# Optimization experiments

Hardware: AMD Instinct MI355X
Metric: run time of the kernel (lower is better)

The kernel has to match this reference:

```python
import jax, jax.numpy as jnp
import numpy as np

H = 128   # hidden_size
DYN = 2   # dynamic_features


def setup_inputs() -> dict:
    B, S, STAT = 256, 64, 2
    key = jax.random.key(0)
    ks = jax.random.split(key, 9)
    sc = 0.05
    return {
        "static": jax.random.normal(ks[0], (B, STAT, S), jnp.float32),
        "static_embeddings": jax.random.normal(ks[1], (B, H, S), jnp.float32),
        "dynamic": jax.random.uniform(ks[2], (B, DYN, S), jnp.float32),
        # dynamic_embedding: Conv1d(2 -> 128, k=1)
        "dyn_w": jax.random.normal(ks[3], (H, DYN), jnp.float32) * sc,
        "dyn_b": jnp.zeros((H,), jnp.float32),
        # decoder_input_dynamic_embedding: Conv1d(128 -> 128, k=1)
        "in_w": jax.random.normal(ks[4], (H, H), jnp.float32) * sc,
        "in_b": jnp.zeros((H,), jnp.float32),
        # GRU (single layer, batch_first), torch gate order r,z,n
        "w_ih": jax.random.normal(ks[5], (3 * H, H), jnp.float32) * sc,
        "w_hh": jax.random.normal(ks[6], (3 * H, H), jnp.float32) * sc,
        "b_ih": jnp.zeros((3 * H,), jnp.float32),
        "b_hh": jnp.zeros((3 * H,), jnp.float32),
        # DoubleAttention: scores = v . tanh(W [static; dynamic; hidden])
        "W_att": jax.random.normal(ks[7], (H, 3 * H), jnp.float32) * sc,
        "v_att": jax.random.normal(ks[8], (H,), jnp.float32) * sc,
    }


def _pointer_forward(static_embeddings, dynamic, dyn_w, dyn_b, in_w, in_b,
                     w_ih, w_hh, b_ih, b_hh, W_att, v_att):
    B, Hd, S = static_embeddings.shape
    NEG = jnp.asarray(-1e9, static_embeddings.dtype)
    base = jax.random.key(42)

    def gru_cell(x, h):  # torch nn.GRU single step
        gi = x @ w_ih.T + b_ih
        gh = h @ w_hh.T + b_hh
        ir, iz, i_n = jnp.split(gi, 3, axis=-1)
        hr, hz, h_n = jnp.split(gh, 3, axis=-1)
        r = jax.nn.sigmoid(ir + hr)
        z = jax.nn.sigmoid(iz + hz)
        n = jnp.tanh(i_n + r * h_n)
        return (1.0 - z) * n + z * h

    first_mask = jnp.zeros((B, S), static_embeddings.dtype).at[:, 0].set(1.0)

    def step(carry, i):
        dec_in, h, visited, dyn = carry
        # decoder_input_dynamic_embedding: 1x1 conv == per-token linear
        x = dec_in @ in_w.T + in_b                      # [B,H]
        h = gru_cell(x, h)                              # decoder_output == new hidden
        # i==0: only depot (index 0) is selectable; afterwards: unvisited nodes
        mask = jnp.where(i == 0, first_mask, 1.0 - visited)
        dyn_emb = jnp.einsum('bds,hd->bhs', dyn, dyn_w) + dyn_b[None, :, None]
        ctx = jnp.concatenate(
            [static_embeddings, dyn_emb,
             jnp.broadcast_to(h[:, :, None], (B, Hd, S))], axis=1)  # [B,3H,S]
        scores = jnp.einsum('h,bhs->bs', v_att,
                            jnp.tanh(jnp.einsum('hk,bks->bhs', W_att, ctx)))
        logits = jnp.where(mask > 0, scores, NEG)       # -inf on masked positions
        ptr = jax.random.categorical(jax.random.fold_in(base, i), logits)  # sample
        logp = jnp.take_along_axis(jax.nn.log_softmax(logits, -1),
                                   ptr[:, None], axis=1)[:, 0]
        sel = (jnp.arange(S)[None, :] == ptr[:, None]).astype(dyn.dtype)  # [B,S]
        visited = jnp.maximum(visited, sel)
        dyn = dyn * (1.0 - sel)[:, None, :]             # update_dynamic_state
        # original feeds the (conv-transformed) decoder input back to itself
        return (x, h, visited, dyn), (ptr, logp)

    init = (static_embeddings[:, :, 0],                  # decoder_input = emb of node 0
            jnp.zeros((B, Hd), static_embeddings.dtype),  # GRU hidden
            jnp.zeros((B, S), static_embeddings.dtype),   # visited
            dynamic)
    _, (tours, logps) = jax.lax.scan(step, init, jnp.arange(S))
    return tours.T, logps.T  # [B,S], [B,S]


def reference(static, static_embeddings, dynamic, dyn_w, dyn_b, in_w, in_b,
              w_ih, w_hh, b_ih, b_hh, W_att, v_att):
    # dropout layers are identity in eval mode; `static` is only used for logging
    return _pointer_forward(static_embeddings, dynamic, dyn_w, dyn_b, in_w, in_b,
                            w_ih, w_hh, b_ih, b_hh, W_att, v_att)
```

## Files before the change

### kernel.cpp

```cpp
#include <hip/hip_runtime.h>
#include <stdint.h>


#define BN 256
#define SN 64
#define HN 128
#define NEGV (-1.0e9f)
#define TINYF 1.17549435e-38f

#define OFF_A   0
#define OFF_GI  8192
#define OFF_WHC 8192
#define OFF_SET 16384
#define OFF_UT  24832
#define OFF_HC  33280
#define OFF_KK  33536
#define OFF_SV  33664
#define OFF_DY  33792
#define OFF_WD  33920
#define OFF_CV  34176
#define OFF_VS  34304
#define SMEM_FLOATS 34308

#define KA_A   0
#define KA_GI  8192
#define KA_HC  32768
#define KA_FLOATS 33024

#define WS_HG   384
#define WS_NEED ((size_t)(384 + 256 * 64 * 128) * 4)

typedef float v4f __attribute__((ext_vector_type(4)));

struct W8 { v4f a, b, c, d, e, f, g, h; };

__device__ __forceinline__ W8 ldg8_s64(const float* p) {
  W8 r;
  asm volatile(
      "global_load_dwordx4 %0, %8, off\n\t"
      "global_load_dwordx4 %1, %8, off offset:64\n\t"
      "global_load_dwordx4 %2, %8, off offset:128\n\t"
      "global_load_dwordx4 %3, %8, off offset:192\n\t"
      "global_load_dwordx4 %4, %8, off offset:256\n\t"
      "global_load_dwordx4 %5, %8, off offset:320\n\t"
      "global_load_dwordx4 %6, %8, off offset:384\n\t"
      "global_load_dwordx4 %7, %8, off offset:448\n\t"
      "s_waitcnt vmcnt(0)"
      : "=&v"(r.a), "=&v"(r.b), "=&v"(r.c), "=&v"(r.d),
        "=&v"(r.e), "=&v"(r.f), "=&v"(r.g), "=&v"(r.h)
      : "v"(p));
  return r;
}

__device__ __forceinline__ float dot8(const W8& w, const float4* x4) {
  float a0 = 0.f, a1 = 0.f, a2 = 0.f, a3 = 0.f;
  a0 = fmaf(w.a.x, x4[0].x, a0); a1 = fmaf(w.a.y, x4[0].y, a1);
  a2 = fmaf(w.a.z, x4[0].z, a2); a3 = fmaf(w.a.w, x4[0].w, a3);
  a0 = fmaf(w.b.x, x4[1].x, a0); a1 = fmaf(w.b.y, x4[1].y, a1);
  a2 = fmaf(w.b.z, x4[1].z, a2); a3 = fmaf(w.b.w, x4[1].w, a3);
  a0 = fmaf(w.c.x, x4[2].x, a0); a1 = fmaf(w.c.y, x4[2].y, a1);
  a2 = fmaf(w.c.z, x4[2].z, a2); a3 = fmaf(w.c.w, x4[2].w, a3);
  a0 = fmaf(w.d.x, x4[3].x, a0); a1 = fmaf(w.d.y, x4[3].y, a1);
  a2 = fmaf(w.d.z, x4[3].z, a2); a3 = fmaf(w.d.w, x4[3].w, a3);
  a0 = fmaf(w.e.x, x4[4].x, a0); a1 = fmaf(w.e.y, x4[4].y, a1);
  a2 = fmaf(w.e.z, x4[4].z, a2); a3 = fmaf(w.e.w, x4[4].w, a3);
  a0 = fmaf(w.f.x, x4[5].x, a0); a1 = fmaf(w.f.y, x4[5].y, a1);
  a2 = fmaf(w.f.z, x4[5].z, a2); a3 = fmaf(w.f.w, x4[5].w, a3);
  a0 = fmaf(w.g.x, x4[6].x, a0); a1 = fmaf(w.g.y, x4[6].y, a1);
  a2 = fmaf(w.g.z, x4[6].z, a2); a3 = fmaf(w.g.w, x4[6].w, a3);
  a0 = fmaf(w.h.x, x4[7].x, a0); a1 = fmaf(w.h.y, x4[7].y, a1);
  a2 = fmaf(w.h.z, x4[7].z, a2); a3 = fmaf(w.h.w, x4[7].w, a3);
  return (a0 + a1) + (a2 + a3);
}

__device__ __forceinline__ uint32_t rotl32(uint32_t v, int d) {
  return (v << d) | (v >> (32 - d));
}

__device__ __forceinline__ void threefry2x32(uint32_t k0, uint32_t k1,
                                             uint32_t x0, uint32_t x1,
                                             uint32_t& o0, uint32_t& o1) {
  uint32_t ks2 = k0 ^ k1 ^ 0x1BD11BDAu;
  x0 += k0; x1 += k1;
  x0 += x1; x1 = rotl32(x1, 13); x1 ^= x0;
  x0 += x1; x1 = rotl32(x1, 15); x1 ^= x0;
  x0 += x1; x1 = rotl32(x1, 26); x1 ^= x0;
  x0 += x1; x1 = rotl32(x1, 6);  x1 ^= x0;
  x0 += k1; x1 += ks2 + 1u;
  x0 += x1; x1 = rotl32(x1, 17); x1 ^= x0;
  x0 += x1; x1 = rotl32(x1, 29); x1 ^= x0;
  x0 += x1; x1 = rotl32(x1, 16); x1 ^= x0;
  x0 += x1; x1 = rotl32(x1, 24); x1 ^= x0;
  x0 += ks2; x1 += k0 + 2u;
  x0 += x1; x1 = rotl32(x1, 13); x1 ^= x0;
  x0 += x1; x1 = rotl32(x1, 15); x1 ^= x0;
  x0 += x1; x1 = rotl32(x1, 26); x1 ^= x0;
  x0 += x1; x1 = rotl32(x1, 6);  x1 ^= x0;
  x0 += k0; x1 += k1 + 3u;
  x0 += x1; x1 = rotl32(x1, 17); x1 ^= x0;
  x0 += x1; x1 = rotl32(x1, 29); x1 ^= x0;
  x0 += x1; x1 = rotl32(x1, 16); x1 ^= x0;
  x0 += x1; x1 = rotl32(x1, 24); x1 ^= x0;
  x0 += k1; x1 += ks2 + 4u;
  x0 += x1; x1 = rotl32(x1, 13); x1 ^= x0;
  x0 += x1; x1 = rotl32(x1, 15); x1 ^= x0;
  x0 += x1; x1 = rotl32(x1, 26); x1 ^= x0;
  x0 += x1; x1 = rotl32(x1, 6);  x1 ^= x0;
  x0 += ks2; x1 += k0 + 5u;
  o0 = x0; o1 = x1;
}

__device__ __forceinline__ float jax_gumbel(uint32_t k0, uint32_t k1, int j) {
  uint32_t o0, o1;
  threefry2x32(k0, k1, 0u, (uint32_t)j, o0, o1);
  uint32_t bits = o0 ^ o1;
  uint32_t ub = (bits >> 9) | 0x3F800000u;
  float u = __uint_as_float(ub) - 1.0f;
  u = fmaxf(u + TINYF, TINYF);
  return -logf(-logf(u));
}

__device__ __forceinline__ float ftanh(float x) {
  float e = __expf(2.0f * x);
  return (e - 1.0f) * __builtin_amdgcn_rcpf(e + 1.0f);
}

__device__ __forceinline__ float fsig(float x) {
  return __builtin_amdgcn_rcpf(1.0f + __expf(-x));
}

__global__ void k0_dyn(const float* __restrict__ W_att, const float* __restrict__ dyn_w,
                       const float* __restrict__ dyn_b, float* __restrict__ Wd,
                       float* __restrict__ cv) {
  int h = threadIdx.x;
  float w0 = 0.f, w1 = 0.f, cc = 0.f;
  for (int k = 0; k < HN; ++k) {
    float w = W_att[h * 384 + 128 + k];
    w0 = fmaf(w, dyn_w[2 * k + 0], w0);
    w1 = fmaf(w, dyn_w[2 * k + 1], w1);
    cc = fmaf(w, dyn_b[k], cc);
  }
  Wd[2 * h] = w0; Wd[2 * h + 1] = w1; cv[h] = cc;
}

__global__ __launch_bounds__(512)
__attribute__((amdgpu_waves_per_eu(2, 2)))
void kA_front(const float* __restrict__ SE, const float* __restrict__ in_w,
              const float* __restrict__ in_b, const float* __restrict__ w_ih,
              const float* __restrict__ b_ih, const float* __restrict__ w_hh,
              const float* __restrict__ b_hh, float* __restrict__ Hg) {
  extern __shared__ float sm[];
  float* A   = sm + KA_A;
  float* GIl = sm + KA_GI;
  float* HC  = sm + KA_HC;
  int b = blockIdx.x, t = threadIdx.x;

  if (t < 128) HC[t] = SE[b * 8192 + t * 64];
  __syncthreads();

  {
    int ml = t >> 2, ks = t & 3;
    W8 wv = ldg8_s64(in_w + ml * HN + ks * 4);
    float bib = in_b[ml];
    for (int ii = 0; ii < SN; ++ii) {
      const float* xc = HC + (ii & 1) * 128;
      float* xn = HC + ((ii + 1) & 1) * 128;
      float4 x4[8];
#pragma unroll
      for (int q = 0; q < 8; ++q)
        x4[q] = *(const float4*)(xc + q * 16 + ks * 4);
      float s = dot8(wv, x4);
      s += __shfl_xor(s, 1); s += __shfl_xor(s, 2);
      if (ks == 0) {
        float xv = s + bib;
        A[ii * 128 + ml] = xv;
        xn[ml] = xv;
      }
      __syncthreads();
    }
  }

  {
    int r = t & 127, cg = t >> 7;
    const float* xb = A + cg * 16 * 128;
    const float* w0p = w_ih + (r)       * HN;
    const float* w1p = w_ih + (r + 128) * HN;
    const float* w2p = w_ih + (r + 256) * HN;
    float acc[3][16];
#pragma unroll
    for (int g = 0; g < 3; ++g)
#pragma unroll
      for (int i = 0; i < 16; ++i) acc[g][i] = 0.f;
#pragma unroll 1
    for (int k = 0; k < HN; k += 4) {
      float4 w0 = *(const float4*)(w0p + k);
      float4 w1 = *(const float4*)(w1p + k);
      float4 w2 = *(const float4*)(w2p + k);
#pragma unroll
      for (int i = 0; i < 16; ++i) {
        float4 xv = *(const float4*)(xb + i * 128 + k);
        acc[0][i] = fmaf(w0.x, xv.x, acc[0][i]);
        acc[0][i] = fmaf(w0.y, xv.y, acc[0][i]);
        acc[0][i] = fmaf(w0.z, xv.z, acc[0][i]);
        acc[0][i] = fmaf(w0.w, xv.w, acc[0][i]);
        acc[1][i] = fmaf(w1.x, xv.x, acc[1][i]);
        acc[1][i] = fmaf(w1.y, xv.y, acc[1][i]);
        acc[1][i] = fmaf(w1.z, xv.z, acc[1][i]);
        acc[1][i] = fmaf(w1.w, xv.w, acc[1][i]);
        acc[2][i] = fmaf(w2.x, xv.x, acc[2][i]);
        acc[2][i] = fmaf(w2.y, xv.y, acc[2][i]);
        acc[2][i] = fmaf(w2.z, xv.z, acc[2][i]);
        acc[2][i] = fmaf(w2.w, xv.w, acc[2][i]);
      }
    }
    float b0 = b_ih[r], b1 = b_ih[r + 128], b2 = b_ih[r + 256];
#pragma unroll
    for (int i = 0; i < 16; ++i) {
      int n = cg * 16 + i;
      GIl[n * 384 + r]       = acc[0][i] + b0;
      GIl[n * 384 + 128 + r] = acc[1][i] + b1;
      GIl[n * 384 + 256 + r] = acc[2][i] + b2;
    }
    __syncthreads();
  }

  if (t < 256) HC[t] = 0.f;
  __syncthreads();
  {
    int ml = t >> 2, ks = t & 3;
    W8 wv0 = ldg8_s64(w_hh + (ml)       * HN + ks * 4);
    W8 wv1 = ldg8_s64(w_hh + (ml + 128) * HN + ks * 4);
    W8 wv2 = ldg8_s64(w_hh + (ml + 256) * HN + ks * 4);
    float bh0 = b_hh[ml], bh1 = b_hh[ml + 128], bh2 = b_hh[ml + 256];
    float hp = 0.f;
    for (int ii = 0; ii < SN; ++ii) {
      const float* hcr = HC + (ii & 1) * 128;
      float* hcw = HC + ((ii + 1) & 1) * 128;
      float gi0 = 0.f, gi1 = 0.f, gi2 = 0.f;
      if (ks == 0) {
        const float* gr = GIl + ii * 384;
        gi0 = gr[ml]; gi1 = gr[128 + ml]; gi2 = gr[256 + ml];
      }
      float4 x4[8];
#pragma unroll
      for (int q = 0; q < 8; ++q)
        x4[q] = *(const float4*)(hcr + q * 16 + ks * 4);
      float s0 = dot8(wv0, x4);
      float s1 = dot8(wv1, x4);
      float s2 = dot8(wv2, x4);
      s0 += __shfl_xor(s0, 1); s0 += __shfl_xor(s0, 2);
      s1 += __shfl_xor(s1, 1); s1 += __shfl_xor(s1, 2);
      s2 += __shfl_xor(s2, 1); s2 += __shfl_xor(s2, 2);
      if (ks == 0) {
        float r = fsig(gi0 + s0 + bh0);
        float z = fsig(gi1 + s1 + bh1);
        float nn = ftanh(gi2 + r * (s2 + bh2));
        float hn = (1.0f - z) * nn + z * hp;
        hcw[ml] = hn;
        Hg[b * 8192 + ii * 128 + ml] = hn;
        hp = hn;
      }
      __syncthreads();
    }
  }
}

__global__ __launch_bounds__(1024)
void k3_att(const float* __restrict__ SE, const float* __restrict__ dynamic,
            const float* __restrict__ dyn_w, const float* __restrict__ dyn_b,
            const float* __restrict__ W_att, const float* __restrict__ v_att,
            const float* __restrict__ Hg, float* __restrict__ out) {
  extern __shared__ float sm[];
  int b = blockIdx.x, t = threadIdx.x;
  float* A   = sm + OFF_A;
  float* WHC = sm + OFF_WHC;
  float* SET = sm + OFF_SET;
  float* UT  = sm + OFF_UT;
  uint32_t* KK = (uint32_t*)(sm + OFF_KK);
  float* SV  = sm + OFF_SV;
  float* DY  = sm + OFF_DY;
  float* WDs = sm + OFF_WD;
  float* CVs = sm + OFF_CV;

  if (t < 512) {
    int h = t >> 2, ks2 = t & 3;
    const float* wp = W_att + h * 384 + 128 + ks2 * 32;
    float w0 = 0.f, w1 = 0.f, cc = 0.f;
    for (int k = 0; k < 32; ++k) {
      float w = wp[k];
      int kk = ks2 * 32 + k;
      w0 = fmaf(w, dyn_w[2 * kk + 0], w0);
      w1 = fmaf(w, dyn_w[2 * kk + 1], w1);
      cc = fmaf(w, dyn_b[kk], cc);
    }
    w0 += __shfl_xor(w0, 1); w0 += __shfl_xor(w0, 2);
    w1 += __shfl_xor(w1, 1); w1 += __shfl_xor(w1, 2);
    cc += __shfl_xor(cc, 1); cc += __shfl_xor(cc, 2);
    if (ks2 == 0) { WDs[2 * h] = w0; WDs[2 * h + 1] = w1; CVs[h] = cc; }
  } else if (t < 640) {
    int tt = t - 512;
    SV[tt] = 2.0f * v_att[tt];
    DY[tt] = dynamic[b * 128 + tt];
  } else if (t < 704) {
    int tt = t - 640;
    uint32_t o0, o1;
    threefry2x32(0u, 42u, 0u, (uint32_t)tt, o0, o1);
    KK[2 * tt] = o0; KK[2 * tt + 1] = o1;
  } else if (t < 768) {
    int tt = t - 704;
    float v = v_att[tt] + v_att[tt + 64];
#pragma unroll
    for (int off = 32; off > 0; off >>= 1) v += __shfl_xor(v, off);
    if (tt == 0) sm[OFF_VS] = v;
  }
  for (int p = 0; p < 8; ++p)
    A[p * 1024 + t] = Hg[b * 8192 + p * 1024 + t];
  __syncthreads();

  {
    int r = t & 127, cg = t >> 7;
    const float* xb = A + cg * 8 * 128;
    const float* wp = W_att + r * 384 + 256;
    float acc[8];
#pragma unroll
    for (int i = 0; i < 8; ++i) acc[i] = 0.f;
#pragma unroll 1
    for (int k = 0; k < HN; k += 4) {
      float4 w = *(const float4*)(wp + k);
#pragma unroll
      for (int i = 0; i < 8; ++i) {
        float4 xv = *(const float4*)(xb + i * 128 + k);
        acc[i] = fmaf(w.x, xv.x, acc[i]);
        acc[i] = fmaf(w.y, xv.y, acc[i]);
        acc[i] = fmaf(w.z, xv.z, acc[i]);
        acc[i] = fmaf(w.w, xv.w, acc[i]);
      }
    }
#pragma unroll
    for (int i = 0; i < 8; ++i)
      WHC[(cg * 8 + i) * 128 + r] = __expf(2.0f * acc[i]);
    __syncthreads();
  }

  for (int p = 0; p < 8; ++p) {
    int idx = p * 1024 + t;
    int h = idx >> 6, s = idx & 63;
    SET[s * 132 + h] = SE[b * 8192 + idx];
  }
  __syncthreads();

  {
    int r = t & 127, cg = t >> 7;
    const float* xb = SET + cg * 8 * 132;
    const float* wp = W_att + r * 384;
    float acc[8];
#pragma unroll
    for (int i = 0; i < 8; ++i) acc[i] = 0.f;
#pragma unroll 1
    for (int k = 0; k < HN; k += 4) {
      float4 w = *(const float4*)(wp + k);
#pragma unroll
      for (int i = 0; i < 8; ++i) {
        float4 xv = *(const float4*)(xb + i * 132 + k);
        acc[i] = fmaf(w.x, xv.x, acc[i]);
        acc[i] = fmaf(w.y, xv.y, acc[i]);
        acc[i] = fmaf(w.z, xv.z, acc[i]);
        acc[i] = fmaf(w.w, xv.w, acc[i]);
      }
    }
    float wd0 = WDs[2 * r], wd1 = WDs[2 * r + 1], cvv = CVs[r];
#pragma unroll
    for (int i = 0; i < 8; ++i) {
      int n = cg * 8 + i;
      UT[r * 66 + n] =
          __expf(2.0f * (acc[i] + wd0 * DY[n] + wd1 * DY[64 + n] + cvv));
    }
    __syncthreads();
  }

  {
    int s = t & 63, slot = t >> 6;
    float vsum = sm[OFF_VS];
    float acc[4];
#pragma unroll
    for (int j = 0; j < 4; ++j) acc[j] = 0.f;
    for (int h = 0; h < HN; h += 4) {
      float u0 = UT[(h + 0) * 66 + s];
      float u1 = UT[(h + 1) * 66 + s];
      float u2 = UT[(h + 2) * 66 + s];
      float u3 = UT[(h + 3) * 66 + s];
      float4 v4 = *(const float4*)(SV + h);
#pragma unroll
      for (int j = 0; j < 4; ++j) {
        float4 wh = *(const float4*)(WHC + (slot * 4 + j) * 128 + h);
        float a = acc[j];
        float d0 = fmaf(u0, wh.x, 1.0f);
        float d1 = fmaf(u1, wh.y, 1.0f);
        float d2 = fmaf(u2, wh.z, 1.0f);
        float d3 = fmaf(u3, wh.w, 1.0f);
        a = fmaf(v4.x, __builtin_amdgcn_rcpf(d0), a);
        a = fmaf(v4.y, __builtin_amdgcn_rcpf(d1), a);
        a = fmaf(v4.z, __builtin_amdgcn_rcpf(d2), a);
        a = fmaf(v4.w, __builtin_amdgcn_rcpf(d3), a);
        acc[j] = a;
      }
    }
    __syncthreads();
#pragma unroll
    for (int j = 0; j < 4; ++j) A[(slot * 4 + j) * 64 + s] = vsum - acc[j];
    __syncthreads();
  }

  {
    float* G = A + 4096;
    for (int p = 0; p < 4; ++p) {
      int idx = p * 1024 + t;
      int i = idx >> 6;
      G[idx] = jax_gumbel(KK[2 * i], KK[2 * i + 1], b * 64 + (idx & 63));
    }
    __syncthreads();
  }

  if (t < 64) {
    const float* Pl = A;
    const float* Gl = A + 4096;
    int s = t;
    bool visited = false;
    for (int i = 0; i < SN; ++i) {
      float score = Pl[i * 64 + s];
      bool allowed = (i == 0) ? (s == 0) : (!visited);
      float logit = allowed ? score : NEGV;
      float z = logit + Gl[i * 64 + s];
      float bz = z; int bi = s;
      float se = expf(logit);
#pragma unroll
      for (int off = 32; off > 0; off >>= 1) {
        float oz = __shfl_xor(bz, off);
        int oi = __shfl_xor(bi, off);
        float os = __shfl_xor(se, off);
        if (oz > bz || (oz == bz && oi < bi)) { bz = oz; bi = oi; }
        se += os;
      }
      int ptr = bi;
      float chosen = __shfl(logit, ptr);
      float logp = chosen - logf(se);
      if (s == ptr) visited = true;
      if (s == 0) {
        out[b * SN + i] = (float)ptr;
        out[BN * SN + b * SN + i] = logp;
      }
    }
  }
}

__global__ __launch_bounds__(512)
__attribute__((amdgpu_waves_per_eu(2, 2)))
void mega(
    const float* __restrict__ SE, const float* __restrict__ dynamic,
    const float* __restrict__ in_w, const float* __restrict__ in_b,
    const float* __restrict__ w_ih, const float* __restrict__ b_ih,
    const float* __restrict__ w_hh, const float* __restrict__ b_hh,
    const float* __restrict__ W_att, const float* __restrict__ v_att,
    const float* __restrict__ Wd, const float* __restrict__ cv,
    float* __restrict__ out) {
  extern __shared__ float sm[];
  int b = blockIdx.x, t = threadIdx.x;
  float* A   = sm + OFF_A;
  float* GIl = sm + OFF_GI;
  float* WHC = sm + OFF_WHC;
  float* SET = sm + OFF_SET;
  float* UT  = sm + OFF_UT;
  float* HC  = sm + OFF_HC;
  uint32_t* KK = (uint32_t*)(sm + OFF_KK);
  float* SV  = sm + OFF_SV;
  float* DY  = sm + OFF_DY;
  float* WDs = sm + OFF_WD;
  float* CVs = sm + OFF_CV;

  if (t < 64) {
    uint32_t o0, o1;
    threefry2x32(0u, 42u, 0u, (uint32_t)t, o0, o1);
    KK[2 * t] = o0; KK[2 * t + 1] = o1;
  }
  if (t < 128) {
    SV[t]  = v_att[t];
    DY[t]  = dynamic[b * 128 + t];
    CVs[t] = cv[t];
    HC[t]  = SE[b * 8192 + t * 64];
  }
  if (t < 256) WDs[t] = Wd[t];
  __syncthreads();

  {
    int ml = t >> 2, ks = t & 3;
    W8 wv = ldg8_s64(in_w + ml * HN + ks * 4);
    float bib = in_b[ml];
    for (int ii = 0; ii < SN; ++ii) {
      const float* xc = HC + (ii & 1) * 128;
      float* xn = HC + ((ii + 1) & 1) * 128;
      float4 x4[8];
#pragma unroll
      for (int q = 0; q < 8; ++q)
        x4[q] = *(const float4*)(xc + q * 16 + ks * 4);
      float s = dot8(wv, x4);
      s += __shfl_xor(s, 1); s += __shfl_xor(s, 2);
      if (ks == 0) {
        float xv = s + bib;
        A[ii * 128 + ml] = xv;
        xn[ml] = xv;
      }
      __syncthreads();
    }
  }
  {
    int r = t & 127, cg = t >> 7;
    const float* xb = A + cg * 16 * 128;
    const float* w0p = w_ih + (r)       * HN;
    const float* w1p = w_ih + (r + 128) * HN;
    const float* w2p = w_ih + (r + 256) * HN;
    float acc[3][16];
#pragma unroll
    for (int g = 0; g < 3; ++g)
#pragma unroll
      for (int i = 0; i < 16; ++i) acc[g][i] = 0.f;
#pragma unroll 1
    for (int k = 0; k < HN; k += 4) {
      float4 w0 = *(const float4*)(w0p + k);
      float4 w1 = *(const float4*)(w1p + k);
      float4 w2 = *(const float4*)(w2p + k);
#pragma unroll
      for (int i = 0; i < 16; ++i) {
        float4 xv = *(const float4*)(xb + i * 128 + k);
        acc[0][i] = fmaf(w0.x, xv.x, acc[0][i]);
        acc[0][i] = fmaf(w0.y, xv.y, acc[0][i]);
        acc[0][i] = fmaf(w0.z, xv.z, acc[0][i]);
        acc[0][i] = fmaf(w0.w, xv.w, acc[0][i]);
        acc[1][i] = fmaf(w1.x, xv.x, acc[1][i]);
        acc[1][i] = fmaf(w1.y, xv.y, acc[1][i]);
        acc[1][i] = fmaf(w1.z, xv.z, acc[1][i]);
        acc[1][i] = fmaf(w1.w, xv.w, acc[1][i]);
        acc[2][i] = fmaf(w2.x, xv.x, acc[2][i]);
        acc[2][i] = fmaf(w2.y, xv.y, acc[2][i]);
        acc[2][i] = fmaf(w2.z, xv.z, acc[2][i]);
        acc[2][i] = fmaf(w2.w, xv.w, acc[2][i]);
      }
    }
    float b0 = b_ih[r], b1 = b_ih[r + 128], b2 = b_ih[r + 256];
#pragma unroll
    for (int i = 0; i < 16; ++i) {
      int n = cg * 16 + i;
      GIl[n * 384 + r]       = acc[0][i] + b0;
      GIl[n * 384 + 128 + r] = acc[1][i] + b1;
      GIl[n * 384 + 256 + r] = acc[2][i] + b2;
    }
    __syncthreads();
  }
  if (t < 256) HC[t] = 0.f;
  __syncthreads();
  {
    int ml = t >> 2, ks = t & 3;
    W8 wv0 = ldg8_s64(w_hh + (ml)       * HN + ks * 4);
    W8 wv1 = ldg8_s64(w_hh + (ml + 128) * HN + ks * 4);
    W8 wv2 = ldg8_s64(w_hh + (ml + 256) * HN + ks * 4);
    float bh0 = b_hh[ml], bh1 = b_hh[ml + 128], bh2 = b_hh[ml + 256];
    float hp = 0.f;
    for (int ii = 0; ii < SN; ++ii) {
      const float* hcr = HC + (ii & 1) * 128;
      float* hcw = HC + ((ii + 1) & 1) * 128;
      float gi0 = 0.f, gi1 = 0.f, gi2 = 0.f;
      if (ks == 0) {
        const float* gr = GIl + ii * 384;
        gi0 = gr[ml]; gi1 = gr[128 + ml]; gi2 = gr[256 + ml];
      }
      float4 x4[8];
#pragma unroll
      for (int q = 0; q < 8; ++q)
        x4[q] = *(const float4*)(hcr + q * 16 + ks * 4);
      float s0 = dot8(wv0, x4);
      float s1 = dot8(wv1, x4);
      float s2 = dot8(wv2, x4);
      s0 += __shfl_xor(s0, 1); s0 += __shfl_xor(s0, 2);
      s1 += __shfl_xor(s1, 1); s1 += __shfl_xor(s1, 2);
      s2 += __shfl_xor(s2, 1); s2 += __shfl_xor(s2, 2);
      if (ks == 0) {
        float r = fsig(gi0 + s0 + bh0);
        float z = fsig(gi1 + s1 + bh1);
        float nn = ftanh(gi2 + r * (s2 + bh2));
        float hn = (1.0f - z) * nn + z * hp;
        hcw[ml] = hn;
        A[ii * 128 + ml] = hn;
        hp = hn;
      }
      __syncthreads();
    }
  }
  {
    int r = t & 127, cg = t >> 7;
    const float* xb = A + cg * 16 * 128;
    const float* wp = W_att + r * 384 + 256;
    float acc[16];
#pragma unroll
    for (int i = 0; i < 16; ++i) acc[i] = 0.f;
#pragma unroll 1
    for (int k = 0; k < HN; k += 4) {
      float4 w = *(const float4*)(wp + k);
#pragma unroll
      for (int i = 0; i < 16; ++i) {
        float4 xv = *(const float4*)(xb + i * 128 + k);
        acc[i] = fmaf(w.x, xv.x, acc[i]);
        acc[i] = fmaf(w.y, xv.y, acc[i]);
        acc[i] = fmaf(w.z, xv.z, acc[i]);
        acc[i] = fmaf(w.w, xv.w, acc[i]);
      }
    }
#pragma unroll
    for (int i = 0; i < 16; ++i)
      WHC[(cg * 16 + i) * 128 + r] = acc[i];
    __syncthreads();
  }
  for (int p = 0; p < 16; ++p) {
    int idx = p * 512 + t;
    int h = idx >> 6, s = idx & 63;
    SET[s * 132 + h] = SE[b * 8192 + idx];
  }
  __syncthreads();
  {
    int r = t & 127, cg = t >> 7;
    const float* xb = SET + cg * 16 * 132;
    const float* wp = W_att + r * 384;
    float acc[16];
#pragma unroll
    for (int i = 0; i < 16; ++i) acc[i] = 0.f;
#pragma unroll 1
    for (int k = 0; k < HN; k += 4) {
      float4 w = *(const float4*)(wp + k);
#pragma unroll
      for (int i = 0; i < 16; ++i) {
        float4 xv = *(const float4*)(xb + i * 132 + k);
        acc[i] = fmaf(w.x, xv.x, acc[i]);
        acc[i] = fmaf(w.y, xv.y, acc[i]);
        acc[i] = fmaf(w.z, xv.z, acc[i]);
        acc[i] = fmaf(w.w, xv.w, acc[i]);
      }
    }
    float wd0 = WDs[2 * r], wd1 = WDs[2 * r + 1], cvv = CVs[r];
#pragma unroll
    for (int i = 0; i < 16; ++i) {
      int n = cg * 16 + i;
      UT[r * 66 + n] = acc[i] + wd0 * DY[n] + wd1 * DY[64 + n] + cvv;
    }
    __syncthreads();
  }
  {
    int s = t & 63, w = t >> 6;
    float acc[8];
#pragma unroll
    for (int j = 0; j < 8; ++j) acc[j] = 0.f;
    for (int h = 0; h < HN; h += 4) {
      float u0 = UT[(h + 0) * 66 + s];
      float u1 = UT[(h + 1) * 66 + s];
      float u2 = UT[(h + 2) * 66 + s];
      float u3 = UT[(h + 3) * 66 + s];
      float4 v4 = *(const float4*)(SV + h);
#pragma unroll
      for (int j = 0; j < 8; ++j) {
        float4 wh = *(const float4*)(WHC + (w * 8 + j) * 128 + h);
        float a = acc[j];
        a = fmaf(v4.x, ftanh(u0 + wh.x), a);
        a = fmaf(v4.y, ftanh(u1 + wh.y), a);
        a = fmaf(v4.z, ftanh(u2 + wh.z), a);
        a = fmaf(v4.w, ftanh(u3 + wh.w), a);
        acc[j] = a;
      }
    }
    __syncthreads();
#pragma unroll
    for (int j = 0; j < 8; ++j) A[(w * 8 + j) * 64 + s] = acc[j];
    __syncthreads();
  }
  {
    float* G = A + 4096;
    for (int p = 0; p < 8; ++p) {
      int idx = p * 512 + t;
      int i = idx >> 6;
      G[idx] = jax_gumbel(KK[2 * i], KK[2 * i + 1], b * 64 + (idx & 63));
    }
    __syncthreads();
  }
  if (t < 64) {
    const float* Pl = A;
    const float* Gl = A + 4096;
    int s = t;
    bool visited = false;
    for (int i = 0; i < SN; ++i) {
      float score = Pl[i * 64 + s];
      bool allowed = (i == 0) ? (s == 0) : (!visited);
      float logit = allowed ? score : NEGV;
      float z = logit + Gl[i * 64 + s];
      float bz = z; int bi = s;
#pragma unroll
      for (int off = 32; off > 0; off >>= 1) {
        float oz = __shfl_xor(bz, off);
        int oi = __shfl_xor(bi, off);
        if (oz > bz || (oz == bz && oi < bi)) { bz = oz; bi = oi; }
      }
      int ptr = bi;
      float m = logit;
#pragma unroll
      for (int off = 32; off > 0; off >>= 1) m = fmaxf(m, __shfl_xor(m, off));
      float e = expf(logit - m);
      float sum = e;
#pragma unroll
      for (int off = 32; off > 0; off >>= 1) sum += __shfl_xor(sum, off);
      float chosen = __shfl(logit, ptr);
      float logp = (chosen - m) - logf(sum);
      if (s == ptr) visited = true;
      if (s == 0) {
        out[b * SN + i] = (float)ptr;
        out[BN * SN + b * SN + i] = logp;
      }
    }
  }
}

extern "C" void kernel_launch(void* const* d_in, const int* in_sizes, int n_in,
                              void* d_out, int out_size, void* d_ws, size_t ws_size,
                              hipStream_t stream) {
  const float* SE    = (const float*)d_in[1];
  const float* dynam = (const float*)d_in[2];
  const float* dyn_w = (const float*)d_in[3];
  const float* dyn_b = (const float*)d_in[4];
  const float* in_w  = (const float*)d_in[5];
  const float* in_b  = (const float*)d_in[6];
  const float* w_ih  = (const float*)d_in[7];
  const float* w_hh  = (const float*)d_in[8];
  const float* b_ih2 = (const float*)d_in[9];
  const float* b_hh  = (const float*)d_in[10];
  const float* W_att = (const float*)d_in[11];
  const float* v_att = (const float*)d_in[12];
  float* out = (float*)d_out;
  float* ws = (float*)d_ws;

  (void)hipFuncSetAttribute((const void*)mega,
                            hipFuncAttributeMaxDynamicSharedMemorySize,
                            SMEM_FLOATS * 4);
  (void)hipFuncSetAttribute((const void*)kA_front,
                            hipFuncAttributeMaxDynamicSharedMemorySize,
                            KA_FLOATS * 4);
  (void)hipFuncSetAttribute((const void*)k3_att,
                            hipFuncAttributeMaxDynamicSharedMemorySize,
                            SMEM_FLOATS * 4);

  if (ws_size >= WS_NEED) {
    float* Hg = ws + WS_HG;
    hipLaunchKernelGGL(kA_front, dim3(BN), dim3(512), KA_FLOATS * 4, stream,
                       SE, in_w, in_b, w_ih, b_ih2, w_hh, b_hh, Hg);
    hipLaunchKernelGGL(k3_att, dim3(BN), dim3(1024), SMEM_FLOATS * 4, stream,
                       SE, dynam, dyn_w, dyn_b, W_att, v_att, Hg, out);
  } else {
    float* Wd = ws;
    float* cv = ws + 256;
    hipLaunchKernelGGL(k0_dyn, dim3(1), dim3(128), 0, stream,
                       W_att, dyn_w, dyn_b, Wd, cv);
    hipLaunchKernelGGL(mega, dim3(BN), dim3(512), SMEM_FLOATS * 4, stream,
                       SE, dynam, in_w, in_b, w_ih, b_ih2, w_hh, b_hh,
                       W_att, v_att, Wd, cv, out);
  }
}
```

Baseline: 280.3 us.

## Widen GRU front kernel to 1024 threads and split gate matvecs across threads

The front kernel now launches 1024 threads per block instead of 512. The serial input-projection and hidden-state recurrences split each row's dot product across more lanes, and the three hidden gates are spread over separate thread groups that write partial results to a small shared buffer. The aim is to shorten the per-step critical path of the sequential GRU recurrence by doing less dot-product work per thread. In exchange it adds an extra block barrier per recurrence step, more shuffle reductions, and fewer registers per thread.

```diff
diff --git a/kernel.cpp b/kernel.cpp
--- a/kernel.cpp
+++ b/kernel.cpp
@@ -25,7 +25,8 @@
 #define KA_A   0
 #define KA_GI  8192
 #define KA_HC  32768
-#define KA_FLOATS 33024
+#define KA_GT  33024
+#define KA_FLOATS 33408
 
 #define WS_HG   384
 #define WS_NEED ((size_t)(384 + 256 * 64 * 128) * 4)
@@ -143,8 +144,7 @@
   Wd[2 * h] = w0; Wd[2 * h + 1] = w1; cv[h] = cc;
 }
 
-__global__ __launch_bounds__(512)
-__attribute__((amdgpu_waves_per_eu(2, 2)))
+__global__ __launch_bounds__(1024, 4)
 void kA_front(const float* __restrict__ SE, const float* __restrict__ in_w,
               const float* __restrict__ in_b, const float* __restrict__ w_ih,
               const float* __restrict__ b_ih, const float* __restrict__ w_hh,
@@ -153,24 +153,38 @@
   float* A   = sm + KA_A;
   float* GIl = sm + KA_GI;
   float* HC  = sm + KA_HC;
+  float* GT  = sm + KA_GT;
   int b = blockIdx.x, t = threadIdx.x;
 
   if (t < 128) HC[t] = SE[b * 8192 + t * 64];
   __syncthreads();
 
   {
-    int ml = t >> 2, ks = t & 3;
-    W8 wv = ldg8_s64(in_w + ml * HN + ks * 4);
+    int ml = t >> 3, ks = t & 7;
+    const float* wp = in_w + ml * HN + ks * 16;
+    float4 w0 = *(const float4*)(wp);
+    float4 w1 = *(const float4*)(wp + 4);
+    float4 w2 = *(const float4*)(wp + 8);
+    float4 w3 = *(const float4*)(wp + 12);
     float bib = in_b[ml];
     for (int ii = 0; ii < SN; ++ii) {
       const float* xc = HC + (ii & 1) * 128;
       float* xn = HC + ((ii + 1) & 1) * 128;
-      float4 x4[8];
-#pragma unroll
-      for (int q = 0; q < 8; ++q)
-        x4[q] = *(const float4*)(xc + q * 16 + ks * 4);
-      float s = dot8(wv, x4);
-      s += __shfl_xor(s, 1); s += __shfl_xor(s, 2);
+      float4 x0 = *(const float4*)(xc + ks * 16);
+      float4 x1 = *(const float4*)(xc + ks * 16 + 4);
+      float4 x2 = *(const float4*)(xc + ks * 16 + 8);
+      float4 x3 = *(const float4*)(xc + ks * 16 + 12);
+      float a0 = 0.f, a1 = 0.f;
+      a0 = fmaf(w0.x, x0.x, a0); a1 = fmaf(w0.y, x0.y, a1);
+      a0 = fmaf(w0.z, x0.z, a0); a1 = fmaf(w0.w, x0.w, a1);
+      a0 = fmaf(w1.x, x1.x, a0); a1 = fmaf(w1.y, x1.y, a1);
+      a0 = fmaf(w1.z, x1.z, a0); a1 = fmaf(w1.w, x1.w, a1);
+      a0 = fmaf(w2.x, x2.x, a0); a1 = fmaf(w2.y, x2.y, a1);
+      a0 = fmaf(w2.z, x2.z, a0); a1 = fmaf(w2.w, x2.w, a1);
+      a0 = fmaf(w3.x, x3.x, a0); a1 = fmaf(w3.y, x3.y, a1);
+      a0 = fmaf(w3.z, x3.z, a0); a1 = fmaf(w3.w, x3.w, a1);
+      float s = a0 + a1;
+      s += __shfl_xor(s, 1); s += __shfl_xor(s, 2); s += __shfl_xor(s, 4);
       if (ks == 0) {
         float xv = s + bib;
         A[ii * 128 + ml] = xv;
@@ -182,22 +196,22 @@
 
   {
     int r = t & 127, cg = t >> 7;
-    const float* xb = A + cg * 16 * 128;
+    const float* xb = A + cg * 8 * 128;
     const float* w0p = w_ih + (r)       * HN;
     const float* w1p = w_ih + (r + 128) * HN;
     const float* w2p = w_ih + (r + 256) * HN;
-    float acc[3][16];
+    float acc[3][8];
 #pragma unroll
     for (int g = 0; g < 3; ++g)
 #pragma unroll
-      for (int i = 0; i < 16; ++i) acc[g][i] = 0.f;
+      for (int i = 0; i < 8; ++i) acc[g][i] = 0.f;
 #pragma unroll 1
     for (int k = 0; k < HN; k += 4) {
       float4 w0 = *(const float4*)(w0p + k);
       float4 w1 = *(const float4*)(w1p + k);
       float4 w2 = *(const float4*)(w2p + k);
 #pragma unroll
-      for (int i = 0; i < 16; ++i) {
+      for (int i = 0; i < 8; ++i) {
         float4 xv = *(const float4*)(xb + i * 128 + k);
         acc[0][i] = fmaf(w0.x, xv.x, acc[0][i]);
         acc[0][i] = fmaf(w0.y, xv.y, acc[0][i]);
@@ -215,8 +229,8 @@
     }
     float b0 = b_ih[r], b1 = b_ih[r + 128], b2 = b_ih[r + 256];
 #pragma unroll
-    for (int i = 0; i < 16; ++i) {
-      int n = cg * 16 + i;
+    for (int i = 0; i < 8; ++i) {
+      int n = cg * 8 + i;
       GIl[n * 384 + r]       = acc[0][i] + b0;
       GIl[n * 384 + 128 + r] = acc[1][i] + b1;
       GIl[n * 384 + 256 + r] = acc[2][i] + b2;
@@ -227,37 +241,64 @@
   if (t < 256) HC[t] = 0.f;
   __syncthreads();
   {
-    int ml = t >> 2, ks = t & 3;
-    W8 wv0 = ldg8_s64(w_hh + (ml)       * HN + ks * 4);
-    W8 wv1 = ldg8_s64(w_hh + (ml + 128) * HN + ks * 4);
-    W8 wv2 = ldg8_s64(w_hh + (ml + 256) * HN + ks * 4);
-    float bh0 = b_hh[ml], bh1 = b_hh[ml + 128], bh2 = b_hh[ml + 256];
+    int g = t >> 9;
+    int ml = (t >> 2) & 127;
+    int ks = t & 3;
+    int row = g * 128 + ml;
+    int mln = t >> 3;
+    int ksn = t & 7;
+
+    W8 wv = ldg8_s64(w_hh + row * HN + ks * 4);
+    float brz = b_hh[row];
+    const float* wnp = w_hh + (256 + mln) * HN + ksn * 16;
+    float4 wn0 = *(const float4*)(wnp);
+    float4 wn1 = *(const float4*)(wnp + 4);
+    float4 wn2 = *(const float4*)(wnp + 8);
+    float4 wn3 = *(const float4*)(wnp + 12);
+    float bn = b_hh[256 + mln];
+
     float hp = 0.f;
     for (int ii = 0; ii < SN; ++ii) {
-      const float* hcr = HC + (ii & 1) * 128;
-      float* hcw = HC + ((ii + 1) & 1) * 128;
+      const float* hc = HC + (ii & 1) * 128;
+      float* hw = HC + ((ii + 1) & 1) * 128;
       float gi0 = 0.f, gi1 = 0.f, gi2 = 0.f;
-      if (ks == 0) {
+      if (t < 128) {
         const float* gr = GIl + ii * 384;
-        gi0 = gr[ml]; gi1 = gr[128 + ml]; gi2 = gr[256 + ml];
+        gi0 = gr[t]; gi1 = gr[128 + t]; gi2 = gr[256 + t];
       }
       float4 x4[8];
 #pragma unroll
       for (int q = 0; q < 8; ++q)
-        x4[q] = *(const float4*)(hcr + q * 16 + ks * 4);
-      float s0 = dot8(wv0, x4);
-      float s1 = dot8(wv1, x4);
-      float s2 = dot8(wv2, x4);
-      s0 += __shfl_xor(s0, 1); s0 += __shfl_xor(s0, 2);
-      s1 += __shfl_xor(s1, 1); s1 += __shfl_xor(s1, 2);
-      s2 += __shfl_xor(s2, 1); s2 += __shfl_xor(s2, 2);
-      if (ks == 0) {
-        float r = fsig(gi0 + s0 + bh0);
-        float z = fsig(gi1 + s1 + bh1);
-        float nn = ftanh(gi2 + r * (s2 + bh2));
+        x4[q] = *(const float4*)(hc + q * 16 + ks * 4);
+      float s = dot8(wv, x4);
+      s += __shfl_xor(s, 1); s += __shfl_xor(s, 2);
+      float4 y0 = *(const float4*)(hc + ksn * 16);
+      float4 y1 = *(const float4*)(hc + ksn * 16 + 4);
+      float4 y2 = *(const float4*)(hc + ksn * 16 + 8);
+      float4 y3 = *(const float4*)(hc + ksn * 16 + 12);
+      float n0 = 0.f, n1 = 0.f;
+      n0 = fmaf(wn0.x, y0.x, n0); n1 = fmaf(wn0.y, y0.y, n1);
+      n0 = fmaf(wn0.z, y0.z, n0); n1 = fmaf(wn0.w, y0.w, n1);
+      n0 = fmaf(wn1.x, y1.x, n0); n1 = fmaf(wn1.y, y1.y, n1);
+      n0 = fmaf(wn1.z, y1.z, n0); n1 = fmaf(wn1.w, y1.w, n1);
+      n0 = fmaf(wn2.x, y2.x, n0); n1 = fmaf(wn2.y, y2.y, n1);
+      n0 = fmaf(wn2.z, y2.z, n0); n1 = fmaf(wn2.w, y2.w, n1);
+      n0 = fmaf(wn3.x, y3.x, n0); n1 = fmaf(wn3.y, y3.y, n1);
+      n0 = fmaf(wn3.z, y3.z, n0); n1 = fmaf(wn3.w, y3.w, n1);
+      float sn = n0 + n1;
+      sn += __shfl_xor(sn, 1); sn += __shfl_xor(sn, 2); sn += __shfl_xor(sn, 4);
+
+      if (ks == 0)  GT[row] = s + brz;
+      if (ksn == 0) GT[256 + mln] = sn + bn;
+      __syncthreads();
+
+      if (t < 128) {
+        float r = fsig(gi0 + GT[t]);
+        float z = fsig(gi1 + GT[128 + t]);
+        float nn = ftanh(gi2 + r * GT[256 + t]);
         float hn = (1.0f - z) * nn + z * hp;
-        hcw[ml] = hn;
-        Hg[b * 8192 + ii * 128 + ml] = hn;
+        hw[t] = hn;
+        Hg[b * 8192 + ii * 128 + t] = hn;
         hp = hn;
       }
       __syncthreads();
@@ -753,7 +794,7 @@
 
   if (ws_size >= WS_NEED) {
     float* Hg = ws + WS_HG;
-    hipLaunchKernelGGL(kA_front, dim3(BN), dim3(512), KA_FLOATS * 4, stream,
+    hipLaunchKernelGGL(kA_front, dim3(BN), dim3(1024), KA_FLOATS * 4, stream,
                        SE, in_w, in_b, w_ih, b_ih2, w_hh, b_hh, Hg);
     hipLaunchKernelGGL(k3_att, dim3(BN), dim3(1024), SMEM_FLOATS * 4, stream,
                        SE, dynam, dyn_w, dyn_b, W_att, v_att, Hg, out);
```

Result: slower. 350.2 us (+25.0%).
